# Kernel tuning notes

Measured on AMD Instinct MI355X. Metric: run time of the kernel, lower is better.

Reference implementation:

```python
import jax, jax.numpy as jnp
import numpy as np
import math

V, L, H, D, T_MAX, FF = 50257, 12, 12, 768, 1024, 3072
B, T = 2, 1024
HD = D // H


def layernorm(x, g, b, eps=1e-5):
    m = x.mean(-1, keepdims=True)
    v = ((x - m) ** 2).mean(-1, keepdims=True)
    return (x - m) / jnp.sqrt(v + eps) * g + b


def mgelu(x):
    # note: module uses 0.047715 (not the standard 0.044715)
    return 0.5 * x * (1.0 + jnp.tanh(math.sqrt(2.0 / math.pi) * (x + 0.047715 * x ** 3)))


def setup_inputs() -> dict:
    key = jax.random.key(0)
    ks = jax.random.split(key, 16)
    s = 0.02
    sr = 0.02 * (2 * L) ** -0.5  # residual-projection init per GPT2 paper
    inp = {
        "idx": jax.random.randint(ks[0], (B, T), 0, V),
        "targets": jax.random.randint(ks[1], (B, T), 0, V),
        "wte": jax.random.normal(ks[2], (V, D), jnp.float32) * s,
        "wpe": jax.random.normal(ks[3], (T_MAX, D), jnp.float32) * s,
        "ln1_g": jnp.ones((L, D), jnp.float32),
        "ln1_b": jnp.zeros((L, D), jnp.float32),
        "qkv_w": jax.random.normal(ks[4], (L, D, 3 * D), jnp.float32) * s,
        "qkv_b": jnp.zeros((L, 3 * D), jnp.float32),
        "po_w": jax.random.normal(ks[5], (L, D, D), jnp.float32) * sr,
        "po_b": jnp.zeros((L, D), jnp.float32),
        "ln2_g": jnp.ones((L, D), jnp.float32),
        "ln2_b": jnp.zeros((L, D), jnp.float32),
        "fc_w": jax.random.normal(ks[6], (L, D, FF), jnp.float32) * s,
        "fc_b": jnp.zeros((L, FF), jnp.float32),
        "pr_w": jax.random.normal(ks[7], (L, FF, D), jnp.float32) * sr,
        "pr_b": jnp.zeros((L, D), jnp.float32),
        "lnf_g": jnp.ones((D,), jnp.float32),
        "lnf_b": jnp.zeros((D,), jnp.float32),
        "lm_w": jax.random.normal(ks[8], (D, V), jnp.float32) * s,
    }
    return inp


def gpt_forward(idx, targets, wte, wpe, ln1_g, ln1_b, qkv_w, qkv_b, po_w, po_b,
                ln2_g, ln2_b, fc_w, fc_b, pr_w, pr_b, lnf_g, lnf_b, lm_w):
    Bt, Tt = idx.shape
    x = wte[idx] + wpe[:Tt]  # [B,T,D]
    causal = jnp.tril(jnp.ones((Tt, Tt), bool))
    scale = 1.0 / math.sqrt(HD)

    def block(x, p):
        g1, b1, wq, bq, wo, bo, g2, b2, wf, bf, wp, bp = p
        h = layernorm(x, g1, b1)
        qkv = h @ wq + bq  # [B,T,3D]
        q, k, v = jnp.split(qkv, 3, axis=-1)
        q = q.reshape(Bt, Tt, H, HD)
        k = k.reshape(Bt, Tt, H, HD)
        v = v.reshape(Bt, Tt, H, HD)
        att = jnp.einsum('bqhd,bkhd->bhqk', q, k) * scale
        att = jnp.where(causal, att, -jnp.inf)
        att = jax.nn.softmax(att, axis=-1)  # dropout = identity (eval)
        y = jnp.einsum('bhqk,bkhd->bqhd', att, v).reshape(Bt, Tt, D)
        x = x + y @ wo + bo
        h2 = layernorm(x, g2, b2)
        x = x + mgelu(h2 @ wf + bf) @ wp + bp
        return x, None

    x, _ = jax.lax.scan(block, x, (ln1_g, ln1_b, qkv_w, qkv_b, po_w, po_b,
                                   ln2_g, ln2_b, fc_w, fc_b, pr_w, pr_b))
    x = layernorm(x, lnf_g, lnf_b)
    logits = x @ lm_w  # [B,T,V]

    logp = jax.nn.log_softmax(logits, axis=-1)
    valid = targets >= 0  # ignore_index=-1
    tgt = jnp.where(valid, targets, 0)
    nll = -jnp.take_along_axis(logp, tgt[..., None], axis=-1)[..., 0]
    loss = (nll * valid).sum() / valid.sum()
    return logits, loss


def reference(idx, targets, wte, wpe, ln1_g, ln1_b, qkv_w, qkv_b, po_w, po_b,
              ln2_g, ln2_b, fc_w, fc_b, pr_w, pr_b, lnf_g, lnf_b, lm_w):
    return gpt_forward(idx, targets, wte, wpe, ln1_g, ln1_b, qkv_w, qkv_b, po_w, po_b,
                       ln2_g, ln2_b, fc_w, fc_b, pr_w, pr_b, lnf_g, lnf_b, lm_w)
```

## Files before the change

### kernel.cpp

```cpp
#include <hip/hip_runtime.h>
#include <hip/hip_bf16.h>
#include <math.h>

#define VOC 50257
#define NL 12
#define NH 12
#define DM 768
#define FF 3072
#define BB 2
#define TT 1024
#define MR (BB*TT)

typedef __attribute__((ext_vector_type(8))) short bf16x8;
typedef __attribute__((ext_vector_type(4))) float f32x4;

__device__ __forceinline__ float mgelu_f(float x) {
    return 0.5f*x*(1.f + tanhf(0.7978845608028654f*(x + 0.047715f*x*x*x)));
}

__device__ __forceinline__ unsigned short f2bf(float f) {
    __hip_bfloat16 h = __float2bfloat16(f);
    return *reinterpret_cast<unsigned short*>(&h);
}

#define GLDS(gptr, lptr) __builtin_amdgcn_global_load_lds( \
    (const __attribute__((address_space(1))) void*)(gptr), \
    (__attribute__((address_space(3))) void*)(lptr), 16, 0, 0)

__device__ __forceinline__ int xcd_work(int bid, int total) {
    int xcd = bid & 7;
    int seq = bid >> 3;
    int q = total >> 3, r = total & 7;
    int base = (xcd < r) ? xcd*(q+1) : r + xcd*q;
    return base + seq;
}

__global__ void embed_kernel(const int* __restrict__ idx, const float* __restrict__ wte,
                             const float* __restrict__ wpe, float* __restrict__ x) {
    int row = blockIdx.x;
    int t = row % TT;
    int tok = idx[row];
    for (int d = threadIdx.x; d < DM; d += blockDim.x)
        x[(size_t)row*DM + d] = wte[(size_t)tok*DM + d] + wpe[(size_t)t*DM + d];
}

__global__ __launch_bounds__(256) void ln_kernel(const float* __restrict__ x,
                          const float* __restrict__ g,
                          const float* __restrict__ b, __hip_bfloat16* __restrict__ out) {
    int row = blockIdx.x*4 + (threadIdx.x >> 6);
    int lane = threadIdx.x & 63;
    const float* xr = x + (size_t)row*DM;
    float vals[DM/64];
    float s = 0.f;
    #pragma unroll
    for (int i = 0; i < DM/64; i++) { vals[i] = xr[lane + i*64]; s += vals[i]; }
    #pragma unroll
    for (int off = 32; off > 0; off >>= 1) s += __shfl_xor(s, off);
    float mean = s * (1.0f/DM);
    float vs = 0.f;
    #pragma unroll
    for (int i = 0; i < DM/64; i++) { float d = vals[i]-mean; vs += d*d; }
    #pragma unroll
    for (int off = 32; off > 0; off >>= 1) vs += __shfl_xor(vs, off);
    float rstd = rsqrtf(vs * (1.0f/DM) + 1e-5f);
    #pragma unroll
    for (int i = 0; i < DM/64; i++) {
        int d = lane + i*64;
        out[(size_t)row*DM + d] = __float2bfloat16((vals[i]-mean)*rstd*g[d] + b[d]);
    }
}

struct TJob { const float* in; __hip_bfloat16* out; int R, C, cx, tile0; };

__device__ __forceinline__ void trans_one(const TJob& j, int t) {
    __shared__ float tile[32][33];
    int bx = t % j.cx, by = t / j.cx;
    int c0 = bx*32, r0 = by*32;
    int tx = threadIdx.x, ty = threadIdx.y;
    #pragma unroll
    for (int i = ty; i < 32; i += 8) {
        int r = r0 + i, c = c0 + tx;
        tile[i][tx] = (r < j.R && c < j.C) ? j.in[(size_t)r*j.C + c] : 0.f;
    }
    __syncthreads();
    #pragma unroll
    for (int i = ty; i < 32; i += 8) {
        int c = c0 + i, r = r0 + tx;
        if (c < j.C && r < j.R) j.out[(size_t)c*j.R + r] = __float2bfloat16(tile[tx][i]);
    }
}

__global__ void trans4_kernel(TJob j0, TJob j1, TJob j2, TJob j3) {
    int t = blockIdx.x;
    if (t >= j3.tile0)      trans_one(j3, t - j3.tile0);
    else if (t >= j2.tile0) trans_one(j2, t - j2.tile0);
    else if (t >= j1.tile0) trans_one(j1, t - j1.tile0);
    else                    trans_one(j0, t);
}

__global__ void trans1_kernel(TJob j0) { trans_one(j0, blockIdx.x); }

template<int MODE, int HALFM>
__global__ __launch_bounds__(256) void mfma_gemm_kernel(
        const __hip_bfloat16* __restrict__ A,
        const __hip_bfloat16* __restrict__ Wt,
        const float* __restrict__ bias,
        const float* __restrict__ res,
        void* __restrict__ Cout,
        __hip_bfloat16* __restrict__ vt,
        int M, int N, int K) {
    constexpr int BM = HALFM ? 64 : 128;
    constexpr int NF = HALFM ? 2 : 4;
    constexpr int ABYTES = 2*BM*64;
    __shared__ __align__(16) char smem[ABYTES + 16384];
    char* As = smem;
    char* Bs = smem + ABYTES;
    int tid = threadIdx.x;
    int lane = tid & 63, wid = tid >> 6;
    int kq = lane >> 4, lr = lane & 15;

    int nby = M / BM;
    int work = xcd_work(blockIdx.x, gridDim.x);
    int by = work % nby;
    int bx = work / nby;
    int m0 = by * BM, n0 = bx * 128;

    int wm = HALFM ? 0 : (wid >> 1);
    int wn = HALFM ? wid : (wid & 1);
    int colbase = HALFM ? wn*32 : wn*64;

    f32x4 acc[4][NF] = {};

    auto STAGE = [&](int buf, int k0) {
        if constexpr (HALFM) {
            GLDS(A + (size_t)(m0 + lane)*K + k0 + wid*8, As + buf*(BM*64) + wid*1024);
            #pragma unroll
            for (int t = 0; t < 2; t++) {
                int lx = wid + t*4;
                int r  = (lx & 1)*64 + lane;
                int kk = (lx >> 1)*8;
                int nr = n0 + r; if (nr > N-1) nr = N-1;
                GLDS(Wt + (size_t)nr*K + k0 + kk, Bs + buf*8192 + lx*1024);
            }
        } else {
            #pragma unroll
            for (int t = 0; t < 2; t++) {
                int lx = wid + t*4;
                int r  = (lx & 1)*64 + lane;
                int kk = (lx >> 1)*8;
                GLDS(A + (size_t)(m0 + r)*K + k0 + kk, As + buf*(BM*64) + lx*1024);
                int nr = n0 + r; if (nr > N-1) nr = N-1;
                GLDS(Wt + (size_t)nr*K + k0 + kk, Bs + buf*8192 + lx*1024);
            }
        }
    };

    int nk = K >> 5;
    STAGE(0, 0);
    __syncthreads();
    for (int ki = 0; ki < nk; ++ki) {
        int cur = ki & 1;
        if (ki + 1 < nk) STAGE(cur ^ 1, (ki+1)*32);

        bf16x8 afrag[4], bfrag[NF];
        #pragma unroll
        for (int m = 0; m < 4; m++)
            afrag[m] = *(const bf16x8*)(As + cur*(BM*64) + kq*(BM*16) + (wm*64 + m*16 + lr)*16);
        #pragma unroll
        for (int n = 0; n < NF; n++)
            bfrag[n] = *(const bf16x8*)(Bs + cur*8192 + kq*2048 + (colbase + n*16 + lr)*16);
        #pragma unroll
        for (int m = 0; m < 4; m++)
            #pragma unroll
            for (int n = 0; n < NF; n++)
                acc[m][n] = __builtin_amdgcn_mfma_f32_16x16x32_bf16(afrag[m], bfrag[n], acc[m][n], 0, 0, 0);
        __syncthreads();
    }

    if (MODE == 0) {
        float* eps = (float*)smem;
        #pragma unroll
        for (int hh = 0; hh < 2; ++hh) {
            __syncthreads();
            if (wn == hh) {
                #pragma unroll
                for (int m = 0; m < 4; m++)
                    #pragma unroll
                    for (int n = 0; n < 4; n++) {
                        int cl = n*16 + lr;
                        #pragma unroll
                        for (int j = 0; j < 4; j++)
                            eps[(wm*64 + m*16 + kq*4 + j)*64 + cl] = acc[m][n][j];
                    }
            }
            __syncthreads();
            #pragma unroll
            for (int it = 0; it < 8; ++it) {
                int rl = it*16 + (tid >> 4);
                int c4 = tid & 15;
                int col = n0 + hh*64 + c4*4;
                int row = m0 + rl;
                f32x4 v = *(const f32x4*)(eps + rl*64 + c4*4);
                if (col + 3 < N) {
                    *(f32x4*)&((float*)Cout)[(size_t)row*N + col] = v;
                } else {
                    #pragma unroll
                    for (int u = 0; u < 4; ++u)
                        if (col + u < N) ((float*)Cout)[(size_t)row*N + col + u] = v[u];
                }
            }
        }
        return;
    }

    #pragma unroll
    for (int m = 0; m < 4; m++) {
        #pragma unroll
        for (int n = 0; n < NF; n++) {
            int col = n0 + colbase + n*16 + lr;
            if (col >= N) continue;
            float bv = bias[col];
            #pragma unroll
            for (int j = 0; j < 4; j++) {
                int row = m0 + wm*64 + m*16 + kq*4 + j;
                float v = acc[m][n][j] + bv;
                size_t o = (size_t)row*N + col;
                if (MODE == 1) {
                    __hip_bfloat16 bvv = __float2bfloat16(v);
                    ((__hip_bfloat16*)Cout)[o] = bvv;
                    if (col >= 2*DM) {
                        int hh = (col - 2*DM) >> 6, dd = (col - 2*DM) & 63;
                        int bb = row >> 10, tt = row & 1023;
                        vt[(((size_t)bb*NH + hh)*64 + dd)*TT + tt] = bvv;
                    }
                } else if (MODE == 2) {
                    ((float*)Cout)[o] = v + res[o];
                } else {
                    ((__hip_bfloat16*)Cout)[o] = __float2bfloat16(mgelu_f(v));
                }
            }
        }
    }
}

__global__ __launch_bounds__(256) void mfma_attn_kernel(const __hip_bfloat16* __restrict__ qkv,
                                                        const __hip_bfloat16* __restrict__ vt,
                                                        __hip_bfloat16* __restrict__ y) {
    __shared__ __align__(16) char K_lds[2][8192];
    __shared__ __align__(16) char VT_lds[2][8192];
    __shared__ __align__(16) char P_lds[4][2048];

    int work = xcd_work(blockIdx.x, BB*NH*16);
    int qt = 15 - (work & 15);
    int bh = work >> 4;
    int h  = bh % NH;
    int b  = bh / NH;
    int tid = threadIdx.x;
    int lane = tid & 63, w = tid >> 6;
    int lr = lane & 15, kq = lane >> 4;
    int q0 = qt * 64;

    int sr = lane >> 3;
    int scb = (lane & 7) * 16;

    int qrow = q0 + w*16 + lr;
    const __hip_bfloat16* qp = qkv + (size_t)(b*TT + qrow)*3*DM + h*64;
    bf16x8 qfrag[2];
    qfrag[0] = *(const bf16x8*)(qp + kq*8);
    qfrag[1] = *(const bf16x8*)(qp + 32 + kq*8);

    f32x4 oacc[4] = {};
    float m_run = -INFINITY, l_run = 0.f;
    const float scale = 0.125f;

    const char* kbase  = (const char*)qkv + ((size_t)b*TT*3*DM + DM + h*64)*2;
    const char* vtbase = (const char*)vt + ((size_t)(b*NH + h)*64)*TT*2;

    auto STAGE = [&](int buf, int kt) {
        int kv0 = kt*64;
        #pragma unroll
        for (int t = 0; t < 2; t++) {
            int lx = w + t*4;
            int r = lx*8 + sr;
            int cbs = scb ^ ((r & 7) << 4);
            GLDS(kbase + (size_t)(kv0 + r)*3*DM*2 + cbs, K_lds[buf] + lx*1024);
            GLDS(vtbase + (size_t)r*TT*2 + kv0*2 + cbs, VT_lds[buf] + lx*1024);
        }
    };

    STAGE(0, 0);
    __syncthreads();
    for (int kt = 0; kt <= qt; ++kt) {
        int cur = kt & 1;
        if (kt < qt) STAGE(cur ^ 1, kt + 1);

        f32x4 st[4] = {};
        #pragma unroll
        for (int t = 0; t < 4; ++t) {
            #pragma unroll
            for (int ks = 0; ks < 2; ++ks) {
                int row = t*16 + lr;
                bf16x8 kf = *(const bf16x8*)(K_lds[cur] + row*128 + ((ks*64 + kq*16) ^ ((lr&7)<<4)));
                st[t] = __builtin_amdgcn_mfma_f32_16x16x32_bf16(kf, qfrag[ks], st[t], 0,0,0);
            }
        }

        float sv[4][4];
        bool diag = (kt == qt);
        float pmax = -INFINITY;
        #pragma unroll
        for (int t = 0; t < 4; ++t)
            #pragma unroll
            for (int jj = 0; jj < 4; ++jj) {
                float s = st[t][jj] * scale;
                if (diag && (t*16 + kq*4 + jj > w*16 + lr)) s = -INFINITY;
                sv[t][jj] = s;
                pmax = fmaxf(pmax, s);
            }
        pmax = fmaxf(pmax, __shfl_xor(pmax, 16));
        pmax = fmaxf(pmax, __shfl_xor(pmax, 32));
        float m_new = fmaxf(m_run, pmax);
        float corr = __expf(m_run - m_new);
        float rsum = 0.f;
        #pragma unroll
        for (int t = 0; t < 4; ++t)
            #pragma unroll
            for (int jj = 0; jj < 4; ++jj) {
                float p = __expf(sv[t][jj] - m_new);
                sv[t][jj] = p;
                rsum += p;
            }
        rsum += __shfl_xor(rsum, 16);
        rsum += __shfl_xor(rsum, 32);
        l_run = l_run * corr + rsum;
        m_run = m_new;

        #pragma unroll
        for (int jj = 0; jj < 4; ++jj) {
            float c = __shfl(corr, kq*20 + jj);
            #pragma unroll
            for (int nt = 0; nt < 4; ++nt) oacc[nt][jj] *= c;
        }

        #pragma unroll
        for (int t = 0; t < 4; ++t) {
            unsigned pk0 = (unsigned)f2bf(sv[t][0]) | ((unsigned)f2bf(sv[t][1]) << 16);
            unsigned pk1 = (unsigned)f2bf(sv[t][2]) | ((unsigned)f2bf(sv[t][3]) << 16);
            unsigned off = ((unsigned)(lr*128 + t*32 + kq*8)) ^ (((unsigned)lr&7u)<<4);
            *(uint2*)(P_lds[w] + off) = make_uint2(pk0, pk1);
        }

        #pragma unroll
        for (int ks = 0; ks < 2; ++ks) {
            bf16x8 pa = *(const bf16x8*)(P_lds[w] +
                ((unsigned)(lr*128 + ((ks*64 + kq*16) ^ ((lr&7)<<4)))));
            #pragma unroll
            for (int nt = 0; nt < 4; ++nt) {
                int row = nt*16 + lr;
                bf16x8 vf = *(const bf16x8*)(VT_lds[cur] + row*128 + ((ks*64 + kq*16) ^ ((lr&7)<<4)));
                oacc[nt] = __builtin_amdgcn_mfma_f32_16x16x32_bf16(pa, vf, oacc[nt], 0,0,0);
            }
        }
        __syncthreads();
    }

    #pragma unroll
    for (int jj = 0; jj < 4; ++jj) {
        float li = __shfl(l_run, kq*20 + jj);
        int qg = q0 + w*16 + kq*4 + jj;
        #pragma unroll
        for (int nt = 0; nt < 4; ++nt)
            y[(size_t)(b*TT + qg)*DM + h*64 + nt*16 + lr] =
                __float2bfloat16(oacc[nt][jj] / li);
    }
}

__global__ void zero_acc_kernel(float* p) { p[threadIdx.x] = 0.f; }

__global__ __launch_bounds__(256) void loss_kernel(const float* __restrict__ logits,
                                                   const int* __restrict__ targets,
                                                   float* __restrict__ acc) {
    int row = blockIdx.x;
    int tid = threadIdx.x;
    const float* lr = logits + (size_t)row * VOC;
    float m = -INFINITY, s = 0.f;
    for (int c4 = tid; c4 < 12564; c4 += 256) {
        f32x4 v = __builtin_nontemporal_load(&((const f32x4*)lr)[c4]);
        float vm = fmaxf(fmaxf(v[0], v[1]), fmaxf(v[2], v[3]));
        if (vm > m) { s *= __expf(m - vm); m = vm; }
        s += __expf(v[0] - m) + __expf(v[1] - m) + __expf(v[2] - m) + __expf(v[3] - m);
    }
    if (tid == 0) {
        float v = lr[VOC - 1];
        if (v > m) { s *= __expf(m - v); m = v; }
        s += __expf(v - m);
    }
    __shared__ float rm[256], rs[256];
    rm[tid] = m; rs[tid] = s; __syncthreads();
    for (int off = 128; off > 0; off >>= 1) {
        if (tid < off) {
            float m2 = rm[tid+off], s2 = rs[tid+off];
            float M = fmaxf(rm[tid], m2);
            rs[tid] = rs[tid]*__expf(rm[tid]-M) + s2*__expf(m2-M);
            rm[tid] = M;
        }
        __syncthreads();
    }
    if (tid == 0) {
        int tgt = targets[row];
        if (tgt >= 0) {
            float lse = logf(rs[0]) + rm[0];
            atomicAdd(&acc[0], lse - lr[tgt]);
            atomicAdd(&acc[1], 1.f);
        }
    }
}

__global__ void loss_final_kernel(const float* acc, float* out) {
    out[0] = acc[0] / acc[1];
}

static inline TJob mkjob(const float* in, __hip_bfloat16* out, int R, int C, int tile0) {
    TJob j; j.in = in; j.out = out; j.R = R; j.C = C;
    j.cx = (C + 31)/32; j.tile0 = tile0;
    return j;
}

extern "C" void kernel_launch(void* const* d_in, const int* in_sizes, int n_in,
                              void* d_out, int out_size, void* d_ws, size_t ws_size,
                              hipStream_t stream) {
    const int*   idx     = (const int*)  d_in[0];
    const int*   targets = (const int*)  d_in[1];
    const float* wte     = (const float*)d_in[2];
    const float* wpe     = (const float*)d_in[3];
    const float* ln1_g   = (const float*)d_in[4];
    const float* ln1_b   = (const float*)d_in[5];
    const float* qkv_w   = (const float*)d_in[6];
    const float* qkv_b   = (const float*)d_in[7];
    const float* po_w    = (const float*)d_in[8];
    const float* po_b    = (const float*)d_in[9];
    const float* ln2_g   = (const float*)d_in[10];
    const float* ln2_b   = (const float*)d_in[11];
    const float* fc_w    = (const float*)d_in[12];
    const float* fc_b    = (const float*)d_in[13];
    const float* pr_w    = (const float*)d_in[14];
    const float* pr_b    = (const float*)d_in[15];
    const float* lnf_g   = (const float*)d_in[16];
    const float* lnf_b   = (const float*)d_in[17];
    const float* lm_w    = (const float*)d_in[18];

    float* logits = (float*)d_out;

    char* p = (char*)d_ws;
    float* x = (float*)p;                 p += (size_t)MR*DM*4;
    __hip_bfloat16* h    = (__hip_bfloat16*)p; p += (size_t)MR*DM*2;
    __hip_bfloat16* qkvb = (__hip_bfloat16*)p; p += (size_t)MR*3*DM*2;
    __hip_bfloat16* yb   = (__hip_bfloat16*)p; p += (size_t)MR*DM*2;
    __hip_bfloat16* fb   = (__hip_bfloat16*)p; p += (size_t)MR*FF*2;
    __hip_bfloat16* vtb  = (__hip_bfloat16*)p; p += (size_t)BB*NH*64*TT*2;
    __hip_bfloat16* lm_wt  = (__hip_bfloat16*)p; p += (size_t)VOC*DM*2;
    __hip_bfloat16* qkv_wt = (__hip_bfloat16*)p; p += (size_t)3*DM*DM*2;
    __hip_bfloat16* po_wt  = (__hip_bfloat16*)p; p += (size_t)DM*DM*2;
    __hip_bfloat16* fc_wt  = (__hip_bfloat16*)p; p += (size_t)FF*DM*2;
    __hip_bfloat16* pr_wt  = (__hip_bfloat16*)p; p += (size_t)DM*FF*2;
    float* lacc = (float*)p;

    dim3 tpb(32, 8);

    embed_kernel<<<MR, 256, 0, stream>>>(idx, wte, wpe, x);

    {
        TJob j = mkjob(lm_w, lm_wt, DM, VOC, 0);
        int tiles = j.cx * ((DM+31)/32);
        trans1_kernel<<<tiles, tpb, 0, stream>>>(j);
    }

    for (int l = 0; l < NL; l++) {
        TJob j0 = mkjob(qkv_w + (size_t)l*DM*3*DM, qkv_wt, DM, 3*DM, 0);
        int t1 = j0.cx * 24;
        TJob j1 = mkjob(po_w + (size_t)l*DM*DM, po_wt, DM, DM, t1);
        int t2 = t1 + j1.cx * 24;
        TJob j2 = mkjob(fc_w + (size_t)l*DM*FF, fc_wt, DM, FF, t2);
        int t3 = t2 + j2.cx * 24;
        TJob j3 = mkjob(pr_w + (size_t)l*FF*DM, pr_wt, FF, DM, t3);
        int tot = t3 + j3.cx * 96;
        trans4_kernel<<<tot, tpb, 0, stream>>>(j0, j1, j2, j3);

        ln_kernel<<<MR/4, 256, 0, stream>>>(x, ln1_g + l*DM, ln1_b + l*DM, h);
        mfma_gemm_kernel<1,0><<<(3*DM/128)*(MR/128), 256, 0, stream>>>(
            h, qkv_wt, qkv_b + (size_t)l*3*DM, nullptr, qkvb, vtb, MR, 3*DM, DM);
        mfma_attn_kernel<<<BB*NH*(TT/64), 256, 0, stream>>>(qkvb, vtb, yb);
        mfma_gemm_kernel<2,1><<<(DM/128)*(MR/64), 256, 0, stream>>>(
            yb, po_wt, po_b + (size_t)l*DM, x, x, nullptr, MR, DM, DM);
        ln_kernel<<<MR/4, 256, 0, stream>>>(x, ln2_g + l*DM, ln2_b + l*DM, h);
        mfma_gemm_kernel<3,0><<<(FF/128)*(MR/128), 256, 0, stream>>>(
            h, fc_wt, fc_b + (size_t)l*FF, nullptr, fb, nullptr, MR, FF, DM);
        mfma_gemm_kernel<2,1><<<(DM/128)*(MR/64), 256, 0, stream>>>(
            fb, pr_wt, pr_b + (size_t)l*DM, x, x, nullptr, MR, DM, FF);
    }

    ln_kernel<<<MR/4, 256, 0, stream>>>(x, lnf_g, lnf_b, h);
    mfma_gemm_kernel<0,0><<<((VOC+127)/128)*(MR/128), 256, 0, stream>>>(
        h, lm_wt, nullptr, nullptr, logits, nullptr, MR, VOC, DM);

    zero_acc_kernel<<<1, 2, 0, stream>>>(lacc);
    loss_kernel<<<MR, 256, 0, stream>>>(logits, targets, lacc);
    loss_final_kernel<<<1, 1, 0, stream>>>(lacc, logits + (size_t)MR*VOC);
}
```

Measured before the change: 3.126 ms.

## Fuse per-tile online softmax partials into LM-head GEMM epilogue

The LM-head GEMM epilogue now computes a per-row running max and sum-of-exp for each 128-column tile and writes them to a small partials buffer. A lightweight reduce kernel then combines these partials to get the log-sum-exp per row, so the full logits array is no longer re-read. The staging buffer row pitch is padded to 68 to reduce LDS bank conflicts, and logits stores become nontemporal. This adds exp work and LDS reads to the GEMM epilogue plus a workspace buffer.

Result: no change. 3.107 ms (-0.6%).

```diff
diff --git a/kernel.cpp b/kernel.cpp
--- a/kernel.cpp
+++ b/kernel.cpp
@@ -108,11 +108,13 @@
         const float* __restrict__ res,
         void* __restrict__ Cout,
         __hip_bfloat16* __restrict__ vt,
+        float* __restrict__ part,
         int M, int N, int K) {
     constexpr int BM = HALFM ? 64 : 128;
     constexpr int NF = HALFM ? 2 : 4;
     constexpr int ABYTES = 2*BM*64;
-    __shared__ __align__(16) char smem[ABYTES + 16384];
+    constexpr int SMEMB = (MODE == 0) ? 36864 : (ABYTES + 16384);
+    __shared__ __align__(16) char smem[SMEMB];
     char* As = smem;
     char* Bs = smem + ABYTES;
     int tid = threadIdx.x;
@@ -179,6 +181,9 @@
 
     if (MODE == 0) {
         float* eps = (float*)smem;
+        int nbx = (N + 127) >> 7;
+        int rl2 = tid >> 1, sub = tid & 1;
+        float pm = -INFINITY, ps = 0.f;
         #pragma unroll
         for (int hh = 0; hh < 2; ++hh) {
             __syncthreads();
@@ -190,7 +195,7 @@
                         int cl = n*16 + lr;
                         #pragma unroll
                         for (int j = 0; j < 4; j++)
-                            eps[(wm*64 + m*16 + kq*4 + j)*64 + cl] = acc[m][n][j];
+                            eps[(wm*64 + m*16 + kq*4 + j)*68 + cl] = acc[m][n][j];
                     }
             }
             __syncthreads();
@@ -200,16 +205,33 @@
                 int c4 = tid & 15;
                 int col = n0 + hh*64 + c4*4;
                 int row = m0 + rl;
-                f32x4 v = *(const f32x4*)(eps + rl*64 + c4*4);
+                f32x4 v = *(const f32x4*)(eps + rl*68 + c4*4);
                 if (col + 3 < N) {
-                    *(f32x4*)&((float*)Cout)[(size_t)row*N + col] = v;
+                    __builtin_nontemporal_store(v, (f32x4*)&((float*)Cout)[(size_t)row*N + col]);
                 } else {
                     #pragma unroll
                     for (int u = 0; u < 4; ++u)
-                        if (col + u < N) ((float*)Cout)[(size_t)row*N + col + u] = v[u];
+                        if (col + u < N)
+                            __builtin_nontemporal_store(v[u], &((float*)Cout)[(size_t)row*N + col + u]);
                 }
             }
-        }
+            #pragma unroll
+            for (int i = 0; i < 8; ++i) {
+                f32x4 v = *(const f32x4*)(eps + rl2*68 + sub*32 + i*4);
+                #pragma unroll
+                for (int u = 0; u < 4; ++u) {
+                    int col = n0 + hh*64 + sub*32 + i*4 + u;
+                    float xv = (col < N) ? v[u] : -INFINITY;
+                    if (xv > pm) { ps = ps*__expf(pm - xv); pm = xv; ps += 1.f; }
+                    else ps += __expf(xv - pm);
+                }
+            }
+        }
+        float m2 = __shfl_xor(pm, 1), s2 = __shfl_xor(ps, 1);
+        float Mx = fmaxf(pm, m2);
+        float Sx = ps*__expf(pm - Mx) + s2*__expf(m2 - Mx);
+        if (sub == 0)
+            ((float2*)part)[(size_t)(m0 + rl2)*nbx + bx] = make_float2(Mx, Sx);
         return;
     }
 
@@ -377,40 +399,32 @@
 
 __global__ void zero_acc_kernel(float* p) { p[threadIdx.x] = 0.f; }
 
-__global__ __launch_bounds__(256) void loss_kernel(const float* __restrict__ logits,
-                                                   const int* __restrict__ targets,
-                                                   float* __restrict__ acc) {
+__global__ __launch_bounds__(64) void loss_reduce_kernel(const float* __restrict__ part,
+                                                         const float* __restrict__ logits,
+                                                         const int* __restrict__ targets,
+                                                         float* __restrict__ acc) {
     int row = blockIdx.x;
-    int tid = threadIdx.x;
-    const float* lr = logits + (size_t)row * VOC;
+    int lane = threadIdx.x;
+    const int nbx = (VOC + 127) >> 7;
     float m = -INFINITY, s = 0.f;
-    for (int c4 = tid; c4 < 12564; c4 += 256) {
-        f32x4 v = __builtin_nontemporal_load(&((const f32x4*)lr)[c4]);
-        float vm = fmaxf(fmaxf(v[0], v[1]), fmaxf(v[2], v[3]));
-        if (vm > m) { s *= __expf(m - vm); m = vm; }
-        s += __expf(v[0] - m) + __expf(v[1] - m) + __expf(v[2] - m) + __expf(v[3] - m);
-    }
-    if (tid == 0) {
-        float v = lr[VOC - 1];
-        if (v > m) { s *= __expf(m - v); m = v; }
-        s += __expf(v - m);
-    }
-    __shared__ float rm[256], rs[256];
-    rm[tid] = m; rs[tid] = s; __syncthreads();
-    for (int off = 128; off > 0; off >>= 1) {
-        if (tid < off) {
-            float m2 = rm[tid+off], s2 = rs[tid+off];
-            float M = fmaxf(rm[tid], m2);
-            rs[tid] = rs[tid]*__expf(rm[tid]-M) + s2*__expf(m2-M);
-            rm[tid] = M;
-        }
-        __syncthreads();
-    }
-    if (tid == 0) {
+    for (int bx = lane; bx < nbx; bx += 64) {
+        float2 p = ((const float2*)part)[(size_t)row*nbx + bx];
+        float Mx = fmaxf(m, p.x);
+        s = s*__expf(m - Mx) + p.y*__expf(p.x - Mx);
+        m = Mx;
+    }
+    #pragma unroll
+    for (int off = 32; off > 0; off >>= 1) {
+        float m2 = __shfl_xor(m, off), s2 = __shfl_xor(s, off);
+        float Mx = fmaxf(m, m2);
+        s = s*__expf(m - Mx) + s2*__expf(m2 - Mx);
+        m = Mx;
+    }
+    if (lane == 0) {
         int tgt = targets[row];
         if (tgt >= 0) {
-            float lse = logf(rs[0]) + rm[0];
-            atomicAdd(&acc[0], lse - lr[tgt]);
+            float lse = logf(s) + m;
+            atomicAdd(&acc[0], lse - logits[(size_t)row*VOC + tgt]);
             atomicAdd(&acc[1], 1.f);
         }
     }
@@ -463,6 +477,7 @@
     __hip_bfloat16* po_wt  = (__hip_bfloat16*)p; p += (size_t)DM*DM*2;
     __hip_bfloat16* fc_wt  = (__hip_bfloat16*)p; p += (size_t)FF*DM*2;
     __hip_bfloat16* pr_wt  = (__hip_bfloat16*)p; p += (size_t)DM*FF*2;
+    float* part = (float*)p;              p += (size_t)MR*((VOC+127)/128)*2*4;
     float* lacc = (float*)p;
 
     dim3 tpb(32, 8);
@@ -488,22 +503,22 @@
 
         ln_kernel<<<MR/4, 256, 0, stream>>>(x, ln1_g + l*DM, ln1_b + l*DM, h);
         mfma_gemm_kernel<1,0><<<(3*DM/128)*(MR/128), 256, 0, stream>>>(
-            h, qkv_wt, qkv_b + (size_t)l*3*DM, nullptr, qkvb, vtb, MR, 3*DM, DM);
+            h, qkv_wt, qkv_b + (size_t)l*3*DM, nullptr, qkvb, vtb, nullptr, MR, 3*DM, DM);
         mfma_attn_kernel<<<BB*NH*(TT/64), 256, 0, stream>>>(qkvb, vtb, yb);
         mfma_gemm_kernel<2,1><<<(DM/128)*(MR/64), 256, 0, stream>>>(
-            yb, po_wt, po_b + (size_t)l*DM, x, x, nullptr, MR, DM, DM);
+            yb, po_wt, po_b + (size_t)l*DM, x, x, nullptr, nullptr, MR, DM, DM);
         ln_kernel<<<MR/4, 256, 0, stream>>>(x, ln2_g + l*DM, ln2_b + l*DM, h);
         mfma_gemm_kernel<3,0><<<(FF/128)*(MR/128), 256, 0, stream>>>(
-            h, fc_wt, fc_b + (size_t)l*FF, nullptr, fb, nullptr, MR, FF, DM);
+            h, fc_wt, fc_b + (size_t)l*FF, nullptr, fb, nullptr, nullptr, MR, FF, DM);
         mfma_gemm_kernel<2,1><<<(DM/128)*(MR/64), 256, 0, stream>>>(
-            fb, pr_wt, pr_b + (size_t)l*DM, x, x, nullptr, MR, DM, FF);
+            fb, pr_wt, pr_b + (size_t)l*DM, x, x, nullptr, nullptr, MR, DM, FF);
     }
 
     ln_kernel<<<MR/4, 256, 0, stream>>>(x, lnf_g, lnf_b, h);
     mfma_gemm_kernel<0,0><<<((VOC+127)/128)*(MR/128), 256, 0, stream>>>(
-        h, lm_wt, nullptr, nullptr, logits, nullptr, MR, VOC, DM);
+        h, lm_wt, nullptr, nullptr, logits, nullptr, part, MR, VOC, DM);
 
     zero_acc_kernel<<<1, 2, 0, stream>>>(lacc);
-    loss_kernel<<<MR, 256, 0, stream>>>(logits, targets, lacc);
+    loss_reduce_kernel<<<MR, 64, 0, stream>>>(part, logits, targets, lacc);
     loss_final_kernel<<<1, 1, 0, stream>>>(lacc, logits + (size_t)MR*VOC);
 }
```
